# Kernel optimization log

Hardware: AMD Instinct MI355X
Metric: run time of the kernel (lower is better)

The kernel has to match this reference:

```python
import jax, jax.numpy as jnp
import numpy as np

B = 128
N = 65536          # total nodes across batched subgraphs
E = 1048576        # total edges
CLIP_DIM = 768
PD = 512           # projection_dim


def setup_inputs() -> dict:
    key = jax.random.key(0)
    ks = jax.random.split(key, 20)
    s = 0.02
    return {
        # CLIP-encoded features (clip encoders treated as upstream feature extractors)
        "image_features": jax.random.normal(ks[0], (B, CLIP_DIM), jnp.float32),
        "text_features": jax.random.normal(ks[1], (B, CLIP_DIM), jnp.float32),
        "answer": jax.random.uniform(ks[2], (B,), jnp.float32),
        # batched subgraph (X_fixed rows already gathered, as in extract_subgraph_batch)
        "x_nodes": jax.random.normal(ks[3], (N, PD), jnp.float32),
        "edge_index": jax.random.randint(ks[4], (2, E), 0, N, jnp.int32),
        "batch_vec": jnp.sort(jax.random.randint(ks[5], (N,), 0, B, jnp.int32)),
        # image/text projections (clip_dim != projection_dim -> Linear)
        "W_img": jax.random.normal(ks[6], (CLIP_DIM, PD), jnp.float32) * s,
        "b_img": jnp.zeros((PD,), jnp.float32),
        "W_txt": jax.random.normal(ks[7], (CLIP_DIM, PD), jnp.float32) * s,
        "b_txt": jnp.zeros((PD,), jnp.float32),
        # implicit classifier: Linear(2*PD, PD) -> ReLU -> Linear(PD, 1)
        "W1": jax.random.normal(ks[8], (2 * PD, PD), jnp.float32) * s,
        "b1": jnp.zeros((PD,), jnp.float32),
        "W2": jax.random.normal(ks[9], (PD, 1), jnp.float32) * s,
        "b2": jnp.zeros((1,), jnp.float32),
        # GCNConv(PD, PD)
        "Wg": jax.random.normal(ks[10], (PD, PD), jnp.float32) * s,
        "bg": jnp.zeros((PD,), jnp.float32),
        # symbolic classifier: Linear(PD, PD) -> ReLU -> Linear(PD, 1)
        "Ws1": jax.random.normal(ks[11], (PD, PD), jnp.float32) * s,
        "bs1": jnp.zeros((PD,), jnp.float32),
        "Ws2": jax.random.normal(ks[12], (PD, 1), jnp.float32) * s,
        "bs2": jnp.zeros((1,), jnp.float32),
    }


def gcn_conv(x, edge_index, W, b):
    """PyG GCNConv: h = W x; add self-loops; sym-normalized sum aggregation."""
    n = x.shape[0]
    h = x @ W                                     # [N, PD] dense GEMM
    loop = jnp.arange(n, dtype=edge_index.dtype)
    src = jnp.concatenate([edge_index[0], loop])  # [E+N]
    dst = jnp.concatenate([edge_index[1], loop])
    deg = jax.ops.segment_sum(jnp.ones_like(dst, dtype=h.dtype), dst, num_segments=n)
    dis = jax.lax.rsqrt(deg)                      # deg >= 1 (self loops)
    norm = dis[src] * dis[dst]                    # [E+N]
    out = jax.ops.segment_sum(h[src] * norm[:, None], dst, num_segments=n)
    return out + b


def reference(image_features, text_features, answer, x_nodes, edge_index, batch_vec,
              W_img, b_img, W_txt, b_txt, W1, b1, W2, b2,
              Wg, bg, Ws1, bs1, Ws2, bs2):
    # ---- implicit branch (MedicalVQAModel.forward) ----
    img = image_features @ W_img + b_img          # [B, PD]
    txt = text_features @ W_txt + b_txt           # [B, PD]
    combined = jnp.concatenate([img, txt], axis=-1)
    h = jax.nn.relu(combined @ W1 + b1)           # dropout p=0.1 inactive (eval)
    y_implicit = (h @ W2 + b2)[:, 0]              # [B]

    # ---- symbolic branch: GCN over batched subgraphs ----
    x = gcn_conv(x_nodes, edge_index, Wg, bg)
    x = jax.nn.relu(x)                            # dropout p=0.8 inactive (eval)
    bv = batch_vec.astype(jnp.int32)
    sums = jax.ops.segment_sum(x, bv, num_segments=B)          # [B, PD]
    cnts = jax.ops.segment_sum(jnp.ones((x.shape[0],), x.dtype), bv, num_segments=B)
    graph_features = sums / jnp.maximum(cnts, 1.0)[:, None]    # global_mean_pool
    hs = jax.nn.relu(graph_features @ Ws1 + bs1)
    y_symbolic = (hs @ Ws2 + bs2)[:, 0]           # [B]

    logits = jnp.maximum(y_implicit, y_symbolic)
    # BCEWithLogits (mean): log(1+e^l) - l*y
    loss = jnp.mean(jnp.logaddexp(0.0, logits) - logits * answer)
    return (logits, loss)
```

## Files before the change

### kernel.cpp

```cpp
#include <hip/hip_runtime.h>
#include <stdint.h>

#define N_NODES 65536
#define N_EDGES 1048576
#define BATCH   128
#define PD      512
#define CLIPD   768

typedef __attribute__((ext_vector_type(4))) float f32x4;
typedef __attribute__((ext_vector_type(2))) float f32x2;
typedef __attribute__((ext_vector_type(4))) int   i32x4;
typedef __attribute__((ext_vector_type(2))) int   i32x2;

__device__ __forceinline__ unsigned short f2b(float f) {
    uint32_t u = __float_as_uint(f);
    return (unsigned short)((u + 0x7fffu + ((u >> 16) & 1u)) >> 16);
}

__device__ __forceinline__ uint32_t pk_fp4(float x, float y, float one) {
    uint32_t r = 0;
    asm("v_cvt_scalef32_pk_fp4_f32 %0, %1, %2, %3" : "+v"(r) : "v"(x), "v"(y), "v"(one));
    return r;
}
__device__ __forceinline__ f32x2 upk_fp4(uint32_t b, float one) {
    f32x2 r;
    asm("v_cvt_scalef32_pk_f32_fp4 %0, %1, %2" : "=v"(r) : "v"(b), "v"(one));
    return r;
}

__device__ __forceinline__ void gl_lds16(const void* g, void* l) {
    __builtin_amdgcn_global_load_lds((const __attribute__((address_space(1))) void*)g,
                                     (__attribute__((address_space(3))) void*)l, 16, 0, 0);
}

__global__ void k_wgt(const float* __restrict__ Wg, uint8_t* __restrict__ WgT8,
                      const int* __restrict__ bv, int* __restrict__ cnts) {
    __shared__ float tile[32][33];
    int kb = blockIdx.x * 32, nb = blockIdx.y * 32;
    int tx = threadIdx.x, ty = threadIdx.y;
    if (kb == 0 && nb == 0) {
        int tid = ty * 32 + tx;
        if (tid < BATCH) {
            int lo = 0, hi = N_NODES;
            while (lo < hi) { int m = (lo + hi) >> 1; if (bv[m] < tid) lo = m + 1; else hi = m; }
            int lo2 = lo, hi2 = N_NODES;
            while (lo2 < hi2) { int m = (lo2 + hi2) >> 1; if (bv[m] < tid + 1) lo2 = m + 1; else hi2 = m; }
            cnts[tid] = lo2 - lo;
        }
    }
    tile[ty][tx] = Wg[(size_t)(kb + ty) * PD + nb + tx];
    __syncthreads();
    uint32_t p = __builtin_amdgcn_cvt_pk_fp8_f32(32.f * tile[tx][ty], 0.f, 0, false);
    WgT8[(size_t)(nb + ty) * PD + kb + tx] = (uint8_t)p;
}

__global__ void k_deg(const int* __restrict__ ei, int* __restrict__ deg) {
    int e = blockIdx.x * 256 + threadIdx.x;
    atomicAdd(&deg[ei[N_EDGES + e]], 1);
}

__global__ void k_scan(const int* __restrict__ deg, int* __restrict__ row_ptr,
                       float* __restrict__ dis) {
    __shared__ int wsum[16];
    const int t = threadIdx.x;
    const int w = t >> 6, l = t & 63;
    const int base = w * 4096;
    int s = 0;
    for (int i = 0; i < 64; ++i) s += deg[base + i * 64 + l];
#pragma unroll
    for (int off = 1; off < 64; off <<= 1) s += __shfl_xor(s, off);
    if (l == 0) wsum[w] = s;
    __syncthreads();
    int carry = 0;
    for (int i = 0; i < 16; ++i) carry += (i < w) ? wsum[i] : 0;
    int idx = base + l;
    int d = deg[idx];
    for (int i = 0; i < 64; ++i) {
        int dn = 0;
        if (i < 63) dn = deg[idx + 64];
        int v = d;
        int inc = v;
#pragma unroll
        for (int off = 1; off < 64; off <<= 1) {
            int n = __shfl_up(inc, off);
            if (l >= off) inc += n;
        }
        row_ptr[idx] = carry + inc - v;
        dis[idx] = rsqrtf((float)(d + 1));
        carry += __shfl(inc, 63);
        idx += 64;
        d = dn;
    }
    if (t == 1023) row_ptr[N_NODES] = carry;
}

__global__ void k_scatter(const int* __restrict__ ei, const int* __restrict__ row_ptr,
                          int* __restrict__ fill, int* __restrict__ srcs) {
    int e = blockIdx.x * 256 + threadIdx.x;
    int d = ei[N_EDGES + e];
    int pos = row_ptr[d] + atomicAdd(&fill[d], 1);
    srcs[pos] = ei[e];
}

__device__ __forceinline__ void mfma16f8(f32x4& acc, i32x2 a, i32x2 b) {
    asm("v_mfma_f32_16x16x32_fp8_fp8 %0, %1, %2, %0" : "+v"(acc) : "v"(a), "v"(b));
}

__global__ __launch_bounds__(256) void k_gemm(const float* __restrict__ X,
                                              const uint8_t* __restrict__ WgT8,
                                              const float* __restrict__ dis,
                                              uint8_t* __restrict__ hn4) {
    __shared__ __align__(16) uint8_t As[64 * 32];
    __shared__ __align__(16) uint8_t Bs[512 * 32];
    const int m0 = blockIdx.x * 64;
    const int t = threadIdx.x;
    const int lane = t & 63, w = t >> 6;
    const int wr = w >> 1, wc = w & 1;
    const int g = lane >> 4, lr = lane & 15;

    f32x4 acc[2][16] = {};

    for (int k0 = 0; k0 < PD; k0 += 32) {
        __syncthreads();
        {
            int r = t >> 2, kc = (t & 3) * 8;
            const float* xp = &X[(size_t)(m0 + r) * PD + k0 + kc];
            float4 v0 = *(const float4*)xp;
            float4 v1 = *(const float4*)(xp + 4);
            uint32_t p0 = __builtin_amdgcn_cvt_pk_fp8_f32(v0.x, v0.y, 0, false);
            p0 = __builtin_amdgcn_cvt_pk_fp8_f32(v0.z, v0.w, p0, true);
            uint32_t p1 = __builtin_amdgcn_cvt_pk_fp8_f32(v1.x, v1.y, 0, false);
            p1 = __builtin_amdgcn_cvt_pk_fp8_f32(v1.z, v1.w, p1, true);
            uint2 o = {p0, p1};
            *(uint2*)&As[r * 32 + kc] = o;
        }
#pragma unroll
        for (int it = 0; it < 4; ++it) {
            int idx = it * 256 + t;
            int r = idx >> 1, koff = (idx & 1) * 16;
            gl_lds16(&WgT8[(size_t)r * PD + k0 + koff], &Bs[idx * 16]);
        }
        __syncthreads();

        i32x2 a[2], b[16];
#pragma unroll
        for (int i = 0; i < 2; ++i) a[i] = *(const i32x2*)&As[(wr * 32 + i * 16 + lr) * 32 + g * 8];
#pragma unroll
        for (int j = 0; j < 16; ++j) b[j] = *(const i32x2*)&Bs[(wc * 256 + j * 16 + lr) * 32 + g * 8];
#pragma unroll
        for (int i = 0; i < 2; ++i)
#pragma unroll
            for (int j = 0; j < 16; ++j) mfma16f8(acc[i][j], a[i], b[j]);
    }
    asm volatile("s_nop 7\n s_nop 7\n s_nop 7\n s_nop 7");

    const float one = 1.0f;
#pragma unroll
    for (int i = 0; i < 2; ++i) {
#pragma unroll
        for (int r = 0; r < 4; ++r) {
            int row = m0 + wr * 32 + i * 16 + g * 4 + r;
            float dd = dis[row] * 0.5f;
#pragma unroll
            for (int jh = 0; jh < 8; ++jh) {
                float x = acc[i][2 * jh][r] * dd;
                float y = acc[i][2 * jh + 1][r] * dd;
                uint32_t p = pk_fp4(x, y, one);
                hn4[(size_t)row * 256 + (wc * 8 + jh) * 16 + lr] = (uint8_t)p;
            }
        }
    }
}

#define NPB 8
__global__ __launch_bounds__(256) void k_agg(const uint8_t* __restrict__ hn4,
                                             const float* __restrict__ dis,
                                             const float* __restrict__ bg,
                                             const int* __restrict__ row_ptr,
                                             const int* __restrict__ srcs,
                                             const int* __restrict__ bv,
                                             float* __restrict__ sums) {
    const int t = threadIdx.x;
    const int c0 = (t >> 4) * 32 + (t & 15);
    const int c1 = c0 + 16;
    const int node0 = blockIdx.x * NPB;
    const float bg0 = bg[c0], bg1 = bg[c1];
    const float one = 1.0f;
    float s0 = 0.f, s1 = 0.f;
    int curb = bv[node0];
    for (int ni = 0; ni < NPB; ++ni) {
        int node = node0 + ni;
        int b = bv[node];
        if (b != curb) {
            atomicAdd(&sums[(size_t)curb * PD + c0], s0);
            atomicAdd(&sums[(size_t)curb * PD + c1], s1);
            s0 = s1 = 0.f;
            curb = b;
        }
        float a0 = 0.f, a1 = 0.f;
        int beg = row_ptr[node], end = row_ptr[node + 1];
        int e = beg;
        if (e + 16 <= end) {
            int sn[16];
#pragma unroll
            for (int q = 0; q < 16; ++q) sn[q] = srcs[e + q];
            for (; e + 32 <= end; e += 16) {
                int sn2[16];
#pragma unroll
                for (int q = 0; q < 16; ++q) sn2[q] = srcs[e + 16 + q];
                uint32_t v[16];
#pragma unroll
                for (int q = 0; q < 16; ++q) v[q] = hn4[(size_t)sn[q] * 256 + t];
#pragma unroll
                for (int q = 0; q < 16; ++q) {
                    f32x2 f = upk_fp4(v[q], one);
                    a0 += f[0];
                    a1 += f[1];
                }
#pragma unroll
                for (int q = 0; q < 16; ++q) sn[q] = sn2[q];
            }
            {
                uint32_t v[16];
#pragma unroll
                for (int q = 0; q < 16; ++q) v[q] = hn4[(size_t)sn[q] * 256 + t];
#pragma unroll
                for (int q = 0; q < 16; ++q) {
                    f32x2 f = upk_fp4(v[q], one);
                    a0 += f[0];
                    a1 += f[1];
                }
                e += 16;
            }
        }
        for (; e + 8 <= end; e += 8) {
            int sn[8];
#pragma unroll
            for (int q = 0; q < 8; ++q) sn[q] = srcs[e + q];
            uint32_t v[8];
#pragma unroll
            for (int q = 0; q < 8; ++q)
                v[q] = hn4[(size_t)sn[q] * 256 + t];
#pragma unroll
            for (int q = 0; q < 8; ++q) {
                f32x2 f = upk_fp4(v[q], one);
                a0 += f[0];
                a1 += f[1];
            }
        }
        for (; e < end; ++e) {
            f32x2 f = upk_fp4(hn4[(size_t)srcs[e] * 256 + t], one);
            a0 += f[0];
            a1 += f[1];
        }
        {
            f32x2 f = upk_fp4(hn4[(size_t)node * 256 + t], one);
            a0 += f[0];
            a1 += f[1];
        }
        float dd = dis[node] * 0.0625f;
        a0 = fmaxf(fmaf(a0, dd, bg0), 0.f);
        a1 = fmaxf(fmaf(a1, dd, bg1), 0.f);
        s0 += a0;
        s1 += a1;
    }
    atomicAdd(&sums[(size_t)curb * PD + c0], s0);
    atomicAdd(&sums[(size_t)curb * PD + c1], s1);
}

__device__ __forceinline__ void lin_part_core(const float* __restrict__ a,
                                              const float* __restrict__ wp,
                                              float* __restrict__ P, int slot, int c0) {
    float acc0 = 0.f, acc1 = 0.f, acc2 = 0.f, acc3 = 0.f;
    float acc4 = 0.f, acc5 = 0.f, acc6 = 0.f, acc7 = 0.f;
#pragma unroll 4
    for (int k = 0; k < 256; k += 8) {
        float a0 = a[k + 0], a1 = a[k + 1], a2 = a[k + 2], a3 = a[k + 3];
        float a4 = a[k + 4], a5 = a[k + 5], a6 = a[k + 6], a7 = a[k + 7];
        float2 w0 = *(const float2*)&wp[(size_t)(k + 0) * PD];
        float2 w1 = *(const float2*)&wp[(size_t)(k + 1) * PD];
        float2 w2 = *(const float2*)&wp[(size_t)(k + 2) * PD];
        float2 w3 = *(const float2*)&wp[(size_t)(k + 3) * PD];
        float2 w4 = *(const float2*)&wp[(size_t)(k + 4) * PD];
        float2 w5 = *(const float2*)&wp[(size_t)(k + 5) * PD];
        float2 w6 = *(const float2*)&wp[(size_t)(k + 6) * PD];
        float2 w7 = *(const float2*)&wp[(size_t)(k + 7) * PD];
        acc0 = fmaf(a0, w0.x, acc0); acc1 = fmaf(a0, w0.y, acc1);
        acc2 = fmaf(a1, w1.x, acc2); acc3 = fmaf(a1, w1.y, acc3);
        acc4 = fmaf(a2, w2.x, acc4); acc5 = fmaf(a2, w2.y, acc5);
        acc6 = fmaf(a3, w3.x, acc6); acc7 = fmaf(a3, w3.y, acc7);
        acc0 = fmaf(a4, w4.x, acc0); acc1 = fmaf(a4, w4.y, acc1);
        acc2 = fmaf(a5, w5.x, acc2); acc3 = fmaf(a5, w5.y, acc3);
        acc4 = fmaf(a6, w6.x, acc4); acc5 = fmaf(a6, w6.y, acc5);
        acc6 = fmaf(a7, w7.x, acc6); acc7 = fmaf(a7, w7.y, acc7);
    }
    P[(size_t)slot * PD + c0] = (acc0 + acc2) + (acc4 + acc6);
    P[(size_t)slot * PD + c0 + 1] = (acc1 + acc3) + (acc5 + acc7);
}

__global__ __launch_bounds__(256) void k_lin_part(const float* __restrict__ A,
                                                  const float* __restrict__ W,
                                                  float* __restrict__ P, int K) {
    const int row = blockIdx.x, kc = blockIdx.y, c0 = threadIdx.x * 2;
    lin_part_core(A + (size_t)row * K + kc * 256, W + (size_t)kc * 256 * PD + c0,
                  P, row * 8 + kc, c0);
}

__global__ __launch_bounds__(256) void k_lin_part_it(const float* __restrict__ IMG,
                                                     const float* __restrict__ TXT,
                                                     const float* __restrict__ Wi,
                                                     const float* __restrict__ Wt,
                                                     float* __restrict__ P) {
    const int row = blockIdx.x, kc = blockIdx.y, c0 = threadIdx.x * 2;
    const float* A = (kc < 3) ? IMG : TXT;
    const float* W = (kc < 3) ? Wi : Wt;
    const int sub = (kc < 3) ? kc : kc - 3;
    lin_part_core(A + (size_t)row * CLIPD + sub * 256, W + (size_t)sub * 256 * PD + c0,
                  P, row * 8 + kc, c0);
}

__global__ __launch_bounds__(256) void k_lin_red_it(const float* __restrict__ P,
                                                    const float* __restrict__ bi,
                                                    const float* __restrict__ bt,
                                                    float* __restrict__ C) {
    const int row = blockIdx.x, side = blockIdx.y, c0 = threadIdx.x * 2;
    const float* p = P + ((size_t)row * 8 + side * 3) * PD + c0;
    float r0 = p[0] + p[PD] + p[2 * PD];
    float r1 = p[1] + p[PD + 1] + p[2 * PD + 1];
    const float* bias = side ? bt : bi;
    C[(size_t)row * 1024 + side * PD + c0] = r0 + bias[c0];
    C[(size_t)row * 1024 + side * PD + c0 + 1] = r1 + bias[c0 + 1];
}

__global__ __launch_bounds__(256) void k_reddot(const float* __restrict__ P,
                                                const float* __restrict__ bias,
                                                const float* __restrict__ w2,
                                                const float* __restrict__ b2,
                                                float* __restrict__ y,
                                                int nch, const int* __restrict__ cnts) {
    __shared__ float wred[4];
    const int row = blockIdx.x;
    const int t = threadIdx.x;
    const int c0 = t * 2;
    const float* p = P + (size_t)row * 8 * PD + c0;
    float r0 = p[0], r1 = p[1];
    if (nch > 1) { r0 += p[PD];     r1 += p[PD + 1]; }
    if (nch > 2) { r0 += p[2 * PD]; r1 += p[2 * PD + 1]; }
    if (nch > 3) { r0 += p[3 * PD]; r1 += p[3 * PD + 1]; }
    float s = 1.f;
    if (cnts) s = 1.f / fmaxf((float)cnts[row], 1.f);
    r0 = fmaxf(fmaf(r0, s, bias[c0]), 0.f);
    r1 = fmaxf(fmaf(r1, s, bias[c0 + 1]), 0.f);
    float partial = fmaf(r0, w2[c0], r1 * w2[c0 + 1]);
#pragma unroll
    for (int off = 32; off; off >>= 1) partial += __shfl_down(partial, off);
    if ((t & 63) == 0) wred[t >> 6] = partial;
    __syncthreads();
    if (t == 0) y[row] = (wred[0] + wred[1]) + (wred[2] + wred[3]) + b2[0];
}

__global__ void k_final(const float* __restrict__ yi, const float* __restrict__ ys,
                        const float* __restrict__ ans, float* __restrict__ out) {
    __shared__ float red[128];
    int t = threadIdx.x;
    float l = fmaxf(yi[t], ys[t]);
    out[t] = l;
    float li = fmaxf(l, 0.f) + log1pf(expf(-fabsf(l))) - l * ans[t];
    red[t] = li;
    __syncthreads();
    for (int off = 64; off; off >>= 1) {
        if (t < off) red[t] += red[t + off];
        __syncthreads();
    }
    if (t == 0) out[BATCH] = red[0] / (float)BATCH;
}

extern "C" void kernel_launch(void* const* d_in, const int* in_sizes, int n_in,
                              void* d_out, int out_size, void* d_ws, size_t ws_size,
                              hipStream_t stream) {
    const float* image_features = (const float*)d_in[0];
    const float* text_features  = (const float*)d_in[1];
    const float* answer         = (const float*)d_in[2];
    const float* x_nodes        = (const float*)d_in[3];
    const int*   edge_index     = (const int*)d_in[4];
    const int*   batch_vec      = (const int*)d_in[5];
    const float* W_img = (const float*)d_in[6];
    const float* b_img = (const float*)d_in[7];
    const float* W_txt = (const float*)d_in[8];
    const float* b_txt = (const float*)d_in[9];
    const float* W1  = (const float*)d_in[10];
    const float* b1  = (const float*)d_in[11];
    const float* W2  = (const float*)d_in[12];
    const float* b2  = (const float*)d_in[13];
    const float* Wg  = (const float*)d_in[14];
    const float* bg  = (const float*)d_in[15];
    const float* Ws1 = (const float*)d_in[16];
    const float* bs1 = (const float*)d_in[17];
    const float* Ws2 = (const float*)d_in[18];
    const float* bs2 = (const float*)d_in[19];
    float* out = (float*)d_out;

    char* base = (char*)d_ws;
    size_t cur = 0;
    auto alloc = [&](size_t bytes) -> void* {
        void* r = base + cur;
        cur = (cur + bytes + 255) & ~(size_t)255;
        return r;
    };
    uint8_t* WgT8  = (uint8_t*)alloc((size_t)PD * PD);
    uint8_t* hn4   = (uint8_t*)alloc((size_t)N_NODES * 256);
    int*   deg     = (int*)alloc((size_t)N_NODES * 4);
    float* dis     = (float*)alloc((size_t)N_NODES * 4);
    int*   row_ptr = (int*)alloc((size_t)(N_NODES + 1) * 4);
    int*   fill    = (int*)alloc((size_t)N_NODES * 4);
    int*   srcs    = (int*)alloc((size_t)N_EDGES * 4);
    float* sums    = (float*)alloc((size_t)BATCH * PD * 4);
    int*   cnts    = (int*)alloc((size_t)BATCH * 4);
    float* Ppart   = (float*)alloc((size_t)BATCH * 8 * PD * 4);
    float* combined = (float*)alloc((size_t)BATCH * 1024 * 4);
    float* yi      = (float*)alloc((size_t)BATCH * 4);
    float* ys      = (float*)alloc((size_t)BATCH * 4);

    hipMemsetAsync(deg, 0, (size_t)N_NODES * 4, stream);
    hipMemsetAsync(fill, 0, (size_t)N_NODES * 4, stream);
    hipMemsetAsync(sums, 0, (size_t)BATCH * PD * 4, stream);

    hipLaunchKernelGGL(k_wgt, dim3(16, 16), dim3(32, 32), 0, stream, Wg, WgT8, batch_vec, cnts);
    hipLaunchKernelGGL(k_deg, dim3(4096), dim3(256), 0, stream, edge_index, deg);
    hipLaunchKernelGGL(k_scan, dim3(1), dim3(1024), 0, stream, deg, row_ptr, dis);
    hipLaunchKernelGGL(k_scatter, dim3(4096), dim3(256), 0, stream, edge_index, row_ptr, fill, srcs);
    hipLaunchKernelGGL(k_gemm, dim3(N_NODES / 64), dim3(256), 0, stream,
                       x_nodes, WgT8, dis, hn4);
    hipLaunchKernelGGL(k_agg, dim3(N_NODES / NPB), dim3(256), 0, stream,
                       hn4, dis, bg, row_ptr, srcs, batch_vec, sums);

    hipLaunchKernelGGL(k_lin_part_it, dim3(BATCH, 6), dim3(256), 0, stream,
                       image_features, text_features, W_img, W_txt, Ppart);
    hipLaunchKernelGGL(k_lin_red_it, dim3(BATCH, 2), dim3(256), 0, stream,
                       Ppart, b_img, b_txt, combined);
    hipLaunchKernelGGL(k_lin_part, dim3(BATCH, 4), dim3(256), 0, stream,
                       combined, W1, Ppart, 1024);
    hipLaunchKernelGGL(k_reddot, dim3(BATCH), dim3(256), 0, stream,
                       Ppart, b1, W2, b2, yi, 4, (const int*)nullptr);

    hipLaunchKernelGGL(k_lin_part, dim3(BATCH, 2), dim3(256), 0, stream,
                       sums, Ws1, Ppart, PD);
    hipLaunchKernelGGL(k_reddot, dim3(BATCH), dim3(256), 0, stream,
                       Ppart, bs1, Ws2, bs2, ys, 2, cnts);

    hipLaunchKernelGGL(k_final, dim3(1), dim3(128), 0, stream, yi, ys, answer, out);
}
```

Measured before the change: 361.4 us.

## Split edge aggregation across four wavefronts with 32-bit fp4 loads and LDS reduction

The aggregation kernel used to have all 256 threads walk every edge of a node, each loading one byte of the packed fp4 row. Now each of the four wavefronts takes every fourth edge, each lane loads four bytes (eight fp4 values) at once, and the partial sums are combined through shared memory before wave 0 applies normalization, bias, ReLU and the pooling atomics. The aim is fewer, wider memory transactions per gathered row and more independent gathers in flight. In exchange it adds two block barriers per node, leaves three waves idle during the epilogue, and drops the deeper explicit prefetch of source indices.

```diff
diff --git a/kernel.cpp b/kernel.cpp
--- a/kernel.cpp
+++ b/kernel.cpp
@@ -173,6 +173,15 @@
 }
 
 #define NPB 8
+__device__ __forceinline__ void dec8(float a[8], uint32_t v, float one) {
+#pragma unroll
+    for (int k = 0; k < 4; ++k) {
+        f32x2 f = upk_fp4(v >> (8 * k), one);
+        a[2 * k] += f[0];
+        a[2 * k + 1] += f[1];
+    }
+}
+
 __global__ __launch_bounds__(256) void k_agg(const uint8_t* __restrict__ hn4,
                                              const float* __restrict__ dis,
                                              const float* __restrict__ bg,
@@ -180,92 +189,82 @@
                                              const int* __restrict__ srcs,
                                              const int* __restrict__ bv,
                                              float* __restrict__ sums) {
+    __shared__ __align__(16) float cmb[3][64][8];
     const int t = threadIdx.x;
-    const int c0 = (t >> 4) * 32 + (t & 15);
-    const int c1 = c0 + 16;
+    const int w = t >> 6, l = t & 63;
     const int node0 = blockIdx.x * NPB;
-    const float bg0 = bg[c0], bg1 = bg[c1];
     const float one = 1.0f;
-    float s0 = 0.f, s1 = 0.f;
+    int cols[4];
+    float bgv[8];
+#pragma unroll
+    for (int k = 0; k < 4; ++k) {
+        int b = 4 * l + k;
+        cols[k] = ((b >> 4) << 5) + (b & 15);
+        bgv[2 * k] = bg[cols[k]];
+        bgv[2 * k + 1] = bg[cols[k] + 16];
+    }
+    float s[8] = {};
     int curb = bv[node0];
     for (int ni = 0; ni < NPB; ++ni) {
         int node = node0 + ni;
         int b = bv[node];
         if (b != curb) {
-            atomicAdd(&sums[(size_t)curb * PD + c0], s0);
-            atomicAdd(&sums[(size_t)curb * PD + c1], s1);
-            s0 = s1 = 0.f;
+            if (w == 0) {
+#pragma unroll
+                for (int k = 0; k < 4; ++k) {
+                    atomicAdd(&sums[(size_t)curb * PD + cols[k]], s[2 * k]);
+                    atomicAdd(&sums[(size_t)curb * PD + cols[k] + 16], s[2 * k + 1]);
+                }
+            }
+#pragma unroll
+            for (int k = 0; k < 8; ++k) s[k] = 0.f;
             curb = b;
         }
-        float a0 = 0.f, a1 = 0.f;
+        float a[8] = {};
         int beg = row_ptr[node], end = row_ptr[node + 1];
-        int e = beg;
-        if (e + 16 <= end) {
-            int sn[16];
-#pragma unroll
-            for (int q = 0; q < 16; ++q) sn[q] = srcs[e + q];
-            for (; e + 32 <= end; e += 16) {
-                int sn2[16];
-#pragma unroll
-                for (int q = 0; q < 16; ++q) sn2[q] = srcs[e + 16 + q];
-                uint32_t v[16];
-#pragma unroll
-                for (int q = 0; q < 16; ++q) v[q] = hn4[(size_t)sn[q] * 256 + t];
-#pragma unroll
-                for (int q = 0; q < 16; ++q) {
-                    f32x2 f = upk_fp4(v[q], one);
-                    a0 += f[0];
-                    a1 += f[1];
-                }
-#pragma unroll
-                for (int q = 0; q < 16; ++q) sn[q] = sn2[q];
-            }
-            {
-                uint32_t v[16];
-#pragma unroll
-                for (int q = 0; q < 16; ++q) v[q] = hn4[(size_t)sn[q] * 256 + t];
-#pragma unroll
-                for (int q = 0; q < 16; ++q) {
-                    f32x2 f = upk_fp4(v[q], one);
-                    a0 += f[0];
-                    a1 += f[1];
-                }
-                e += 16;
-            }
-        }
-        for (; e + 8 <= end; e += 8) {
-            int sn[8];
-#pragma unroll
-            for (int q = 0; q < 8; ++q) sn[q] = srcs[e + q];
-            uint32_t v[8];
-#pragma unroll
-            for (int q = 0; q < 8; ++q)
-                v[q] = hn4[(size_t)sn[q] * 256 + t];
-#pragma unroll
-            for (int q = 0; q < 8; ++q) {
-                f32x2 f = upk_fp4(v[q], one);
-                a0 += f[0];
-                a1 += f[1];
-            }
-        }
-        for (; e < end; ++e) {
-            f32x2 f = upk_fp4(hn4[(size_t)srcs[e] * 256 + t], one);
-            a0 += f[0];
-            a1 += f[1];
-        }
-        {
-            f32x2 f = upk_fp4(hn4[(size_t)node * 256 + t], one);
-            a0 += f[0];
-            a1 += f[1];
-        }
-        float dd = dis[node] * 0.0625f;
-        a0 = fmaxf(fmaf(a0, dd, bg0), 0.f);
-        a1 = fmaxf(fmaf(a1, dd, bg1), 0.f);
-        s0 += a0;
-        s1 += a1;
-    }
-    atomicAdd(&sums[(size_t)curb * PD + c0], s0);
-    atomicAdd(&sums[(size_t)curb * PD + c1], s1);
+        int e = beg + w;
+        for (; e + 12 < end; e += 16) {
+            int s0 = srcs[e], s1 = srcs[e + 4], s2 = srcs[e + 8], s3 = srcs[e + 12];
+            uint32_t v0 = *(const uint32_t*)&hn4[(size_t)s0 * 256 + 4 * l];
+            uint32_t v1 = *(const uint32_t*)&hn4[(size_t)s1 * 256 + 4 * l];
+            uint32_t v2 = *(const uint32_t*)&hn4[(size_t)s2 * 256 + 4 * l];
+            uint32_t v3 = *(const uint32_t*)&hn4[(size_t)s3 * 256 + 4 * l];
+            dec8(a, v0, one);
+            dec8(a, v1, one);
+            dec8(a, v2, one);
+            dec8(a, v3, one);
+        }
+        for (; e < end; e += 4) {
+            uint32_t v = *(const uint32_t*)&hn4[(size_t)srcs[e] * 256 + 4 * l];
+            dec8(a, v, one);
+        }
+        if (w == 0) {
+            uint32_t v = *(const uint32_t*)&hn4[(size_t)node * 256 + 4 * l];
+            dec8(a, v, one);
+        } else {
+            f32x4 lo = {a[0], a[1], a[2], a[3]};
+            f32x4 hi = {a[4], a[5], a[6], a[7]};
+            *(f32x4*)&cmb[w - 1][l][0] = lo;
+            *(f32x4*)&cmb[w - 1][l][4] = hi;
+        }
+        __syncthreads();
+        if (w == 0) {
+#pragma unroll
+            for (int j = 0; j < 8; ++j)
+                a[j] += (cmb[0][l][j] + cmb[1][l][j]) + cmb[2][l][j];
+            float dd = dis[node] * 0.0625f;
+#pragma unroll
+            for (int j = 0; j < 8; ++j) s[j] += fmaxf(fmaf(a[j], dd, bgv[j]), 0.f);
+        }
+        __syncthreads();
+    }
+    if (w == 0) {
+#pragma unroll
+        for (int k = 0; k < 4; ++k) {
+            atomicAdd(&sums[(size_t)curb * PD + cols[k]], s[2 * k]);
+            atomicAdd(&sums[(size_t)curb * PD + cols[k] + 16], s[2 * k + 1]);
+        }
+    }
 }
 
 __device__ __forceinline__ void lin_part_core(const float* __restrict__ a,
```

Measured after the change: 395.9 us. 9.6% more time.
